# Optimization experiments

Hardware: AMD Instinct MI355X
Metric: run time of the kernel (lower is better)

## Reference

```python
import jax, jax.numpy as jnp
import numpy as np

B, N, C = 2, 1024, 81          # images, proposals/img, classes (class 0 = background)
H, W = 1024, 1024              # image size
D = 100                        # detections_per_img
WX, WY, WW, WH = 10.0, 10.0, 5.0, 5.0   # BoxCoder weights
SCORE_THRESH = 0.05
NMS_THRESH = 0.5
BBOX_XFORM_CLIP = float(np.log(1000.0 / 16.0))
NEG = -1e30
TO_REMOVE = 1.0


def setup_inputs() -> dict:
    key = jax.random.key(0)
    k1, k2, k3, k4 = jax.random.split(key, 4)
    class_logits = jax.random.normal(k1, (B, N, C), jnp.float32)
    regression_outputs = jax.random.normal(k2, (B, N, C * 4), jnp.float32) * 0.5
    # build valid xyxy proposal boxes inside the image
    cxy = jax.random.uniform(k3, (B, N, 2), jnp.float32, 0.0, W - 1.0)
    wh = jax.random.uniform(k4, (B, N, 2), jnp.float32, 8.0, 256.0)
    x1y1 = jnp.clip(cxy - wh / 2, 0.0, W - 1.0)
    x2y2 = jnp.clip(cxy + wh / 2, 0.0, W - 1.0)
    proposals = jnp.concatenate([x1y1, x2y2], axis=-1)
    return dict(class_logits=class_logits,
                regression_outputs=regression_outputs,
                proposals=proposals)


def decode(rel, props):
    # rel: [N, C, 4], props: [N, 4] xyxy -> decoded per-class boxes [N, C, 4], clipped to image
    widths = props[:, 2] - props[:, 0] + TO_REMOVE   # [N]
    heights = props[:, 3] - props[:, 1] + TO_REMOVE
    ctr_x = props[:, 0] + 0.5 * widths
    ctr_y = props[:, 1] + 0.5 * heights
    dx = rel[..., 0] / WX
    dy = rel[..., 1] / WY
    dw = jnp.minimum(rel[..., 2] / WW, BBOX_XFORM_CLIP)
    dh = jnp.minimum(rel[..., 3] / WH, BBOX_XFORM_CLIP)
    pcx = dx * widths[:, None] + ctr_x[:, None]
    pcy = dy * heights[:, None] + ctr_y[:, None]
    pw = jnp.exp(dw) * widths[:, None]
    ph = jnp.exp(dh) * heights[:, None]
    x1 = pcx - 0.5 * pw
    y1 = pcy - 0.5 * ph
    x2 = pcx + 0.5 * pw - 1.0
    y2 = pcy + 0.5 * ph - 1.0
    # clip_to_image
    x1 = jnp.clip(x1, 0.0, W - TO_REMOVE)
    y1 = jnp.clip(y1, 0.0, H - TO_REMOVE)
    x2 = jnp.clip(x2, 0.0, W - TO_REMOVE)
    y2 = jnp.clip(y2, 0.0, H - TO_REMOVE)
    return jnp.stack([x1, y1, x2, y2], axis=-1)


def pairwise_iou(b):
    # b: [N, 4] -> [N, N]
    area = (b[:, 2] - b[:, 0] + TO_REMOVE) * (b[:, 3] - b[:, 1] + TO_REMOVE)
    lt = jnp.maximum(b[:, None, :2], b[None, :, :2])
    rb = jnp.minimum(b[:, None, 2:], b[None, :, 2:])
    wh = jnp.clip(rb - lt + TO_REMOVE, 0.0)
    inter = wh[..., 0] * wh[..., 1]
    return inter / (area[:, None] + area[None, :] - inter)


def nms_keep(boxes, scores):
    # boxes [N,4], scores [N] (NEG for below-threshold boxes) -> keep mask [N] bool
    order = jnp.argsort(-scores)
    b = boxes[order]
    iou = pairwise_iou(b)                       # [N, N]
    valid = scores[order] > NEG / 2             # below-threshold boxes never participate
    idx = jnp.arange(N)

    def body(i, keep):
        sup = keep[i] & (iou[i] > NMS_THRESH) & (idx > i)
        return keep & ~sup

    keep_sorted = jax.lax.fori_loop(0, N, body, valid)
    return jnp.zeros(N, bool).at[order].set(keep_sorted)


def _per_image(logits, rel, props):
    probs = jax.nn.softmax(logits, axis=-1)                 # [N, C]
    boxes = decode(rel.reshape(N, C, 4), props)             # [N, C, 4]
    cls_boxes = jnp.transpose(boxes[:, 1:, :], (1, 0, 2))   # [C-1, N, 4]  (skip background)
    cls_scores = probs[:, 1:].T                              # [C-1, N]
    valid = cls_scores > SCORE_THRESH
    masked_in = jnp.where(valid, cls_scores, NEG)
    keep = jax.vmap(nms_keep)(cls_boxes, masked_in)          # [C-1, N]
    surv = jnp.where(keep & valid, cls_scores, NEG)
    top_scores, top_idx = jax.lax.top_k(surv.reshape(-1), D)  # over (C-1)*N candidates
    cls_idx = top_idx // N
    box_idx = top_idx % N
    sel_boxes = cls_boxes[cls_idx, box_idx]                  # [D, 4]
    labels = cls_idx + 1
    ok = top_scores > NEG / 2
    return (jnp.where(ok[:, None], sel_boxes, 0.0),
            jnp.where(ok, top_scores, 0.0),
            jnp.where(ok, labels, -1))


def reference(class_logits, regression_outputs, proposals):
    # returns (boxes [B,D,4], scores [B,D], labels [B,D]); invalid slots zeroed / label -1
    return jax.vmap(_per_image)(class_logits, regression_outputs, proposals)
```

## Files before the change

### kernel.cpp

```cpp
#include <hip/hip_runtime.h>
#include <math.h>
#include <float.h>

#define BN 2
#define NP 1024
#define NC 81
#define ND 100
#define MAXC 8192
#define CAP2 512
#define CAPT 512
#define NBIN 4096
#define SCORE_T 0.05f
#define NMS_T 0.5f
#define BBOX_CLIP 4.135166556742356f

typedef unsigned long long ull;

__device__ __forceinline__ void decode_box(
    const float* __restrict__ props, const float* __restrict__ regress,
    int b, int n, int c, float& x1, float& y1, float& x2, float& y2)
{
    const float* pr = props + ((size_t)b * NP + n) * 4;
    float p0 = pr[0], p1 = pr[1], p2 = pr[2], p3 = pr[3];
    float w  = p2 - p0 + 1.0f, h = p3 - p1 + 1.0f;
    float cx = p0 + 0.5f * w,  cy = p1 + 0.5f * h;
    const float* rl = regress + (((size_t)b * NP + n) * NC + c) * 4;
    float dx = rl[0] / 10.0f, dy = rl[1] / 10.0f;
    float dw = fminf(rl[2] / 5.0f, BBOX_CLIP);
    float dh = fminf(rl[3] / 5.0f, BBOX_CLIP);
    float pcx = dx * w + cx, pcy = dy * h + cy;
    float pw  = expf(dw) * w, ph = expf(dh) * h;
    x1 = pcx - 0.5f * pw; y1 = pcy - 0.5f * ph;
    x2 = pcx + 0.5f * pw - 1.0f; y2 = pcy + 0.5f * ph - 1.0f;
    x1 = fminf(fmaxf(x1, 0.f), 1023.f);
    y1 = fminf(fmaxf(y1, 0.f), 1023.f);
    x2 = fminf(fmaxf(x2, 0.f), 1023.f);
    y2 = fminf(fmaxf(y2, 0.f), 1023.f);
}

__device__ __forceinline__ void emit_slot(
    float* __restrict__ out, const float* __restrict__ props,
    const float* __restrict__ regress, int b, int d, ull key)
{
    float score = __uint_as_float((unsigned int)(key >> 32));
    float* ob = out + ((size_t)b * ND + d) * 4;
    float* os = out + (size_t)BN * ND * 4 + b * ND + d;
    float* ol = out + (size_t)BN * ND * 5 + b * ND + d;
    if (score > 0.f) {
        unsigned int f = 0xFFFFFFFFu - (unsigned int)(key & 0xFFFFFFFFu);
        int cls = f / NP, n = f % NP;
        float x1, y1, x2, y2;
        decode_box(props, regress, b, n, cls + 1, x1, y1, x2, y2);
        ob[0] = x1; ob[1] = y1; ob[2] = x2; ob[3] = y2;
        *os = score;
        *ol = (float)(cls + 1);
    } else {
        ob[0] = 0.f; ob[1] = 0.f; ob[2] = 0.f; ob[3] = 0.f;
        *os = 0.f;
        *ol = -1.f;
    }
}

__device__ __forceinline__ void bitonic_desc(ull* a, int len, int tid, int nthr)
{
    for (int k = 2; k <= len; k <<= 1) {
        for (int j = k >> 1; j > 0; j >>= 1) {
            for (int i = tid; i < len; i += nthr) {
                int ixj = i ^ j;
                if (ixj > i) {
                    bool desc = ((i & k) == 0);
                    ull x = a[i], y = a[ixj];
                    if (desc ? (x < y) : (x > y)) { a[i] = y; a[ixj] = x; }
                }
            }
            __syncthreads();
        }
    }
}

__global__ __launch_bounds__(256) void softmax_probs_kernel(
    const float* __restrict__ logits, float* __restrict__ probs_t,
    int* __restrict__ cnt, int* __restrict__ done)
{
    int g = blockIdx.x * 256 + threadIdx.x;
    if (g == 0) { cnt[0] = 0; cnt[1] = 0; done[0] = 0; done[1] = 0; }
    if (g >= BN * NP) return;
    int b = g / NP, n = g % NP;
    const float* row = logits + (size_t)g * NC;
    float m = -FLT_MAX;
    for (int i = 0; i < NC; ++i) m = fmaxf(m, row[i]);
    float s = 0.f;
    for (int i = 0; i < NC; ++i) s += expf(row[i] - m);
    for (int c = 1; c < NC; ++c)
        probs_t[((size_t)b * (NC - 1) + (c - 1)) * NP + n] = expf(row[c] - m) / s;
}

__global__ __launch_bounds__(256) void nms_topk_kernel(
    const float* __restrict__ probs_t, const float* __restrict__ regress,
    const float* __restrict__ props, int* __restrict__ cnt, int* __restrict__ done,
    ull* __restrict__ g_key, float* __restrict__ out)
{
    const int tid  = threadIdx.x;
    const int wave = tid >> 6;
    const int l    = tid & 63;
    const int idx  = blockIdx.x;
    const int b    = idx / (NC - 1);
    const int cls  = idx % (NC - 1);
    const int c    = cls + 1;

    __shared__ union {
        struct {
            ull   key[CAP2];
            float x1[CAP2], y1[CAP2], x2[CAP2], y2[CAP2], area[CAP2];
            int   keep[CAP2];
        } a;
        struct {
            int hist[NBIN];
            ull cbuf[CAPT];
        } t;
    } sm;
    __shared__ int s_cnt, s_ret, s_bstar, s_cnt2;

    if (tid == 0) s_cnt = 0;
    __syncthreads();

    const float* prow = probs_t + ((size_t)b * (NC - 1) + cls) * NP;
    float4 v = ((const float4*)prow)[tid];
    #pragma unroll
    for (int q = 0; q < 4; ++q) {
        float p = (&v.x)[q];
        if (p > SCORE_T) {
            int k = atomicAdd(&s_cnt, 1);
            if (k < CAP2) {
                unsigned n = (unsigned)(tid * 4 + q);
                sm.a.key[k] = ((ull)__float_as_uint(p) << 32)
                            | (ull)(0xFFFFFFFFu - n);
            }
        }
    }
    __syncthreads();
    int M = s_cnt; if (M > CAP2) M = CAP2;

    if (M > 64) {
        int Mp = 128; while (Mp < M) Mp <<= 1;
        for (int i = M + tid; i < Mp; i += 256) sm.a.key[i] = 0ull;
        __syncthreads();
        bitonic_desc(sm.a.key, Mp, tid, 256);
        for (int i = tid; i < M; i += 256) {
            int n = (int)(0xFFFFFFFFu - (unsigned)(sm.a.key[i] & 0xFFFFFFFFu));
            float x1, y1, x2, y2;
            decode_box(props, regress, b, n, c, x1, y1, x2, y2);
            sm.a.x1[i] = x1; sm.a.y1[i] = y1; sm.a.x2[i] = x2; sm.a.y2[i] = y2;
            sm.a.area[i] = (x2 - x1 + 1.f) * (y2 - y1 + 1.f);
            sm.a.keep[i] = 1;
        }
        __syncthreads();
        for (int i = 0; i < M; ++i) {
            if (sm.a.keep[i]) {
                float x1i = sm.a.x1[i], y1i = sm.a.y1[i];
                float x2i = sm.a.x2[i], y2i = sm.a.y2[i], ai = sm.a.area[i];
                for (int j = i + 1 + tid; j < M; j += 256) {
                    float lx = fmaxf(x1i, sm.a.x1[j]);
                    float ly = fmaxf(y1i, sm.a.y1[j]);
                    float rx = fminf(x2i, sm.a.x2[j]);
                    float ry = fminf(y2i, sm.a.y2[j]);
                    float wd = fmaxf(rx - lx + 1.f, 0.f);
                    float ht = fmaxf(ry - ly + 1.f, 0.f);
                    float inter = wd * ht;
                    float iou = inter / (ai + sm.a.area[j] - inter);
                    if (iou > NMS_T) sm.a.keep[j] = 0;
                }
            }
            __syncthreads();
        }
        for (int i = tid; i < M; i += 256) {
            if (sm.a.keep[i]) {
                int pos = atomicAdd(&cnt[b], 1);
                if (pos < MAXC) {
                    ull key = sm.a.key[i];
                    unsigned n = 0xFFFFFFFFu - (unsigned)(key & 0xFFFFFFFFu);
                    unsigned f = (unsigned)cls * NP + n;
                    g_key[(size_t)b * MAXC + pos] =
                        (key & 0xFFFFFFFF00000000ull) | (ull)(0xFFFFFFFFu - f);
                }
            }
        }
    } else if (M > 0) {
        if (wave == 0) {
            ull key = (l < M) ? sm.a.key[l] : 0ull;
            #pragma unroll
            for (int k = 2; k <= 64; k <<= 1) {
                #pragma unroll
                for (int j = k >> 1; j > 0; j >>= 1) {
                    ull p = __shfl_xor(key, j, 64);
                    bool lower = (l & j) == 0;
                    bool up    = (l & k) != 0;
                    ull mn = key < p ? key : p;
                    ull mx = key < p ? p : key;
                    key = (lower == up) ? mn : mx;
                }
            }
            float x1 = 0.f, y1 = 0.f, x2 = 0.f, y2 = 0.f, ar = 0.f;
            if (l < M) {
                int n = (int)(0xFFFFFFFFu - (unsigned)(key & 0xFFFFFFFFu));
                decode_box(props, regress, b, n, c, x1, y1, x2, y2);
                ar = (x2 - x1 + 1.f) * (y2 - y1 + 1.f);
            }
            ull keep = (M >= 64) ? ~0ull : ((1ull << M) - 1ull);
            for (int i = 0; i < M; ++i) {
                if ((keep >> i) & 1ull) {
                    float xi1 = __shfl(x1, i, 64), yi1 = __shfl(y1, i, 64);
                    float xi2 = __shfl(x2, i, 64), yi2 = __shfl(y2, i, 64);
                    float ari = __shfl(ar, i, 64);
                    float lx = fmaxf(xi1, x1), ly = fmaxf(yi1, y1);
                    float rx = fminf(xi2, x2), ry = fminf(yi2, y2);
                    float wd = fmaxf(rx - lx + 1.f, 0.f);
                    float ht = fmaxf(ry - ly + 1.f, 0.f);
                    float inter = wd * ht;
                    float iou = inter / (ari + ar - inter);
                    ull sup = __ballot(iou > NMS_T && l > i);
                    keep &= ~sup;
                }
            }
            int nk = __popcll(keep);
            int basep = 0;
            if (l == 0 && nk > 0) basep = atomicAdd(&cnt[b], nk);
            basep = __shfl(basep, 0, 64);
            if ((keep >> l) & 1ull) {
                int pos = basep + __popcll(keep & ((1ull << l) - 1ull));
                if (pos < MAXC) {
                    unsigned n = 0xFFFFFFFFu - (unsigned)(key & 0xFFFFFFFFu);
                    unsigned f = (unsigned)cls * NP + n;
                    g_key[(size_t)b * MAXC + pos] =
                        (key & 0xFFFFFFFF00000000ull) | (ull)(0xFFFFFFFFu - f);
                }
            }
        }
    }

    __syncthreads();
    __threadfence();
    if (tid == 0) s_ret = atomicAdd(&done[b], 1);
    __syncthreads();
    if (s_ret != (NC - 1) - 1) return;
    __threadfence();

    int K = atomicAdd(&cnt[b], 0); if (K > MAXC) K = MAXC;
    ull* keys = g_key + (size_t)b * MAXC;

    for (int i = tid; i < NBIN; i += 256) sm.t.hist[i] = 0;
    if (tid == 0) s_cnt2 = 0;
    __syncthreads();

    for (int i = tid; i < K; i += 256)
        atomicAdd(&sm.t.hist[(int)(keys[i] >> 52)], 1);
    __syncthreads();

    if (tid < 64) {
        int gs = 0;
        for (int q = 0; q < 64; ++q) gs += sm.t.hist[l * 64 + q];
        int pre = gs;
        for (int off = 1; off < 64; off <<= 1) {
            int vv = __shfl_up(pre, off, 64);
            if (l >= off) pre += vv;
        }
        int total = __shfl(pre, 63, 64);
        int S = total - pre + gs;
        ull ball = __ballot(S >= ND);
        int gstar = ball ? (63 - __clzll((long long)ball)) : 0;
        int Sg = __shfl(S, gstar, 64);
        int Gg = __shfl(gs, gstar, 64);
        int A  = Sg - Gg;
        int h  = sm.t.hist[gstar * 64 + l];
        int pre2 = h;
        for (int off = 1; off < 64; off <<= 1) {
            int vv = __shfl_up(pre2, off, 64);
            if (l >= off) pre2 += vv;
        }
        int T = Gg - pre2 + h;
        ull ball2 = __ballot(A + T >= ND);
        int binin = ball2 ? (63 - __clzll((long long)ball2)) : 0;
        if (l == 0) s_bstar = gstar * 64 + binin;
    }
    __syncthreads();
    const int bstar = s_bstar;

    for (int i = tid; i < K; i += 256) {
        ull key = keys[i];
        if ((int)(key >> 52) >= bstar) {
            int p = atomicAdd(&s_cnt2, 1);
            if (p < CAPT) sm.t.cbuf[p] = key;
        }
    }
    __syncthreads();
    const int Tt = s_cnt2;

    if (Tt <= CAPT) {
        int Tp = 128; while (Tp < Tt) Tp <<= 1;
        for (int i = Tt + tid; i < Tp; i += 256) sm.t.cbuf[i] = 0ull;
        __syncthreads();
        bitonic_desc(sm.t.cbuf, Tp, tid, 256);
        for (int d = tid; d < ND; d += 256)
            emit_slot(out, props, regress, b, d, sm.t.cbuf[d]);
    } else {
        ull* rk = sm.a.key;
        int* rp = sm.a.keep;
        for (int d = 0; d < ND; ++d) {
            ull bk = 0ull; int bp = -1;
            for (int t = tid; t < K; t += 256) {
                ull k2 = keys[t];
                if (k2 > bk) { bk = k2; bp = t; }
            }
            rk[tid] = bk; rp[tid] = bp;
            __syncthreads();
            for (int off = 128; off > 0; off >>= 1) {
                if (tid < off && rk[tid + off] > rk[tid]) {
                    rk[tid] = rk[tid + off]; rp[tid] = rp[tid + off];
                }
                __syncthreads();
            }
            if (tid == 0) {
                emit_slot(out, props, regress, b, d, rk[0]);
                if (rp[0] >= 0) keys[rp[0]] = 0ull;
            }
            __syncthreads();
        }
    }
}

extern "C" void kernel_launch(void* const* d_in, const int* in_sizes, int n_in,
                              void* d_out, int out_size, void* d_ws, size_t ws_size,
                              hipStream_t stream) {
    const float* logits  = (const float*)d_in[0];
    const float* regress = (const float*)d_in[1];
    const float* props   = (const float*)d_in[2];
    float* out = (float*)d_out;

    char* ws = (char*)d_ws;
    int*   cnt     = (int*)  (ws);
    int*   done    = (int*)  (ws + 8);
    float* probs_t = (float*)(ws + 256);
    ull*   g_key   = (ull*)  (ws + 256 + (size_t)BN * (NC - 1) * NP * 4);

    hipLaunchKernelGGL(softmax_probs_kernel, dim3(BN * NP / 256), dim3(256), 0, stream,
                       logits, probs_t, cnt, done);
    hipLaunchKernelGGL(nms_topk_kernel, dim3(BN * (NC - 1)), dim3(256), 0, stream,
                       probs_t, regress, props, cnt, done, g_key, out);
}
```

Baseline: 111.1 us.

## Fuse softmax into per-class NMS kernel with fixed slots and flag-based final top-k

Replaces the two-kernel pipeline with one launch. Each class block recomputes the softmax over all of its image's logit rows, staged through shared memory in chunks, and keeps only its own class column. This drops the transposed probability buffer and one kernel launch, at the cost of roughly 80x redundant softmax work and logit reads per image. The global atomic counter is replaced by per-class fixed 64-entry key slots, so survivors beyond 64 per class are silently dropped. The final top-k now runs in the class-0 block, which spins on per-block done flags and adds a single-wave register bitonic sort for up to 256 candidates. The flags are never reset between calls, so a later call can read stale slots from the previous one, and the spin-wait assumes all blocks are co-resident.

```diff
diff --git a/kernel.cpp b/kernel.cpp
--- a/kernel.cpp
+++ b/kernel.cpp
@@ -5,14 +5,18 @@
 #define BN 2
 #define NP 1024
 #define NC 81
+#define NCLS 80
 #define ND 100
-#define MAXC 8192
+#define NSLOT 64
 #define CAP2 512
 #define CAPT 512
 #define NBIN 4096
+#define CHROWS 128
+#define NCHUNK 8
 #define SCORE_T 0.05f
 #define NMS_T 0.5f
 #define BBOX_CLIP 4.135166556742356f
+#define DONE_TAG 0x5A5A5A5A
 
 typedef unsigned long long ull;
 
@@ -78,37 +82,21 @@
     }
 }
 
-__global__ __launch_bounds__(256) void softmax_probs_kernel(
-    const float* __restrict__ logits, float* __restrict__ probs_t,
-    int* __restrict__ cnt, int* __restrict__ done)
-{
-    int g = blockIdx.x * 256 + threadIdx.x;
-    if (g == 0) { cnt[0] = 0; cnt[1] = 0; done[0] = 0; done[1] = 0; }
-    if (g >= BN * NP) return;
-    int b = g / NP, n = g % NP;
-    const float* row = logits + (size_t)g * NC;
-    float m = -FLT_MAX;
-    for (int i = 0; i < NC; ++i) m = fmaxf(m, row[i]);
-    float s = 0.f;
-    for (int i = 0; i < NC; ++i) s += expf(row[i] - m);
-    for (int c = 1; c < NC; ++c)
-        probs_t[((size_t)b * (NC - 1) + (c - 1)) * NP + n] = expf(row[c] - m) / s;
-}
-
-__global__ __launch_bounds__(256) void nms_topk_kernel(
-    const float* __restrict__ probs_t, const float* __restrict__ regress,
-    const float* __restrict__ props, int* __restrict__ cnt, int* __restrict__ done,
+__global__ __launch_bounds__(256) void roihead_kernel(
+    const float* __restrict__ logits, const float* __restrict__ regress,
+    const float* __restrict__ props, int* __restrict__ flags,
     ull* __restrict__ g_key, float* __restrict__ out)
 {
     const int tid  = threadIdx.x;
+    const int l    = tid & 63;
     const int wave = tid >> 6;
-    const int l    = tid & 63;
     const int idx  = blockIdx.x;
-    const int b    = idx / (NC - 1);
-    const int cls  = idx % (NC - 1);
+    const int b    = idx / NCLS;
+    const int cls  = idx % NCLS;
     const int c    = cls + 1;
 
     __shared__ union {
+        float4 stage4[CHROWS * NC / 4];
         struct {
             ull   key[CAP2];
             float x1[CAP2], y1[CAP2], x2[CAP2], y2[CAP2], area[CAP2];
@@ -119,13 +107,28 @@
             ull cbuf[CAPT];
         } t;
     } sm;
-    __shared__ int s_cnt, s_ret, s_bstar, s_cnt2;
-
-    if (tid == 0) s_cnt = 0;
-    __syncthreads();
-
-    const float* prow = probs_t + ((size_t)b * (NC - 1) + cls) * NP;
-    float4 v = ((const float4*)prow)[tid];
+    __shared__ float sp[NP];
+    __shared__ int s_cnt, s_app, s_bstar, s_cnt2;
+
+    const float4* lg4 = (const float4*)(logits + (size_t)b * NP * NC);
+    for (int ch = 0; ch < NCHUNK; ++ch) {
+        const float4* src = lg4 + ch * (CHROWS * NC / 4);
+        for (int i = tid; i < CHROWS * NC / 4; i += 256) sm.stage4[i] = src[i];
+        __syncthreads();
+        if (tid < CHROWS) {
+            const float* row = (const float*)sm.stage4 + tid * NC;
+            float m = -FLT_MAX;
+            for (int i = 0; i < NC; ++i) m = fmaxf(m, row[i]);
+            float s = 0.f;
+            for (int i = 0; i < NC; ++i) s += expf(row[i] - m);
+            sp[ch * CHROWS + tid] = expf(row[c] - m) / s;
+        }
+        __syncthreads();
+    }
+
+    if (tid == 0) { s_cnt = 0; s_app = 0; }
+    __syncthreads();
+    float4 v = ((const float4*)sp)[tid];
     #pragma unroll
     for (int q = 0; q < 4; ++q) {
         float p = (&v.x)[q];
@@ -140,6 +143,7 @@
     }
     __syncthreads();
     int M = s_cnt; if (M > CAP2) M = CAP2;
+    ull* g_slot = g_key + (size_t)idx * NSLOT;
 
     if (M > 64) {
         int Mp = 128; while (Mp < M) Mp <<= 1;
@@ -175,17 +179,20 @@
         }
         for (int i = tid; i < M; i += 256) {
             if (sm.a.keep[i]) {
-                int pos = atomicAdd(&cnt[b], 1);
-                if (pos < MAXC) {
+                int pos = atomicAdd(&s_app, 1);
+                if (pos < NSLOT) {
                     ull key = sm.a.key[i];
                     unsigned n = 0xFFFFFFFFu - (unsigned)(key & 0xFFFFFFFFu);
                     unsigned f = (unsigned)cls * NP + n;
-                    g_key[(size_t)b * MAXC + pos] =
-                        (key & 0xFFFFFFFF00000000ull) | (ull)(0xFFFFFFFFu - f);
-                }
-            }
-        }
-    } else if (M > 0) {
+                    g_slot[pos] = (key & 0xFFFFFFFF00000000ull)
+                                | (ull)(0xFFFFFFFFu - f);
+                }
+            }
+        }
+        __syncthreads();
+        int st = s_app; if (st > NSLOT) st = NSLOT;
+        for (int i = st + tid; i < NSLOT; i += 256) g_slot[i] = 0ull;
+    } else {
         if (wave == 0) {
             ull key = (l < M) ? sm.a.key[l] : 0ull;
             #pragma unroll
@@ -222,38 +229,38 @@
                     keep &= ~sup;
                 }
             }
-            int nk = __popcll(keep);
-            int basep = 0;
-            if (l == 0 && nk > 0) basep = atomicAdd(&cnt[b], nk);
-            basep = __shfl(basep, 0, 64);
+            ull vout = 0ull;
             if ((keep >> l) & 1ull) {
-                int pos = basep + __popcll(keep & ((1ull << l) - 1ull));
-                if (pos < MAXC) {
-                    unsigned n = 0xFFFFFFFFu - (unsigned)(key & 0xFFFFFFFFu);
-                    unsigned f = (unsigned)cls * NP + n;
-                    g_key[(size_t)b * MAXC + pos] =
-                        (key & 0xFFFFFFFF00000000ull) | (ull)(0xFFFFFFFFu - f);
-                }
-            }
+                unsigned n = 0xFFFFFFFFu - (unsigned)(key & 0xFFFFFFFFu);
+                unsigned f = (unsigned)cls * NP + n;
+                vout = (key & 0xFFFFFFFF00000000ull) | (ull)(0xFFFFFFFFu - f);
+            }
+            g_slot[l] = vout;
         }
     }
 
     __syncthreads();
     __threadfence();
-    if (tid == 0) s_ret = atomicAdd(&done[b], 1);
-    __syncthreads();
-    if (s_ret != (NC - 1) - 1) return;
+    if (tid == 0) atomicExch(&flags[idx], DONE_TAG);
+    if (cls != 0) return;
+
+    if (tid < NCLS) {
+        int* fp = flags + b * NCLS + tid;
+        while (atomicAdd(fp, 0) != DONE_TAG) { }
+    }
+    __syncthreads();
     __threadfence();
 
-    int K = atomicAdd(&cnt[b], 0); if (K > MAXC) K = MAXC;
-    ull* keys = g_key + (size_t)b * MAXC;
+    const int K = NCLS * NSLOT;
+    const ull* keys = g_key + (size_t)b * NCLS * NSLOT;
 
     for (int i = tid; i < NBIN; i += 256) sm.t.hist[i] = 0;
     if (tid == 0) s_cnt2 = 0;
     __syncthreads();
-
-    for (int i = tid; i < K; i += 256)
-        atomicAdd(&sm.t.hist[(int)(keys[i] >> 52)], 1);
+    for (int i = tid; i < K; i += 256) {
+        ull key = keys[i];
+        if (key) atomicAdd(&sm.t.hist[(int)(key >> 52)], 1);
+    }
     __syncthreads();
 
     if (tid < 64) {
@@ -287,7 +294,7 @@
 
     for (int i = tid; i < K; i += 256) {
         ull key = keys[i];
-        if ((int)(key >> 52) >= bstar) {
+        if (key && (int)(key >> 52) >= bstar) {
             int p = atomicAdd(&s_cnt2, 1);
             if (p < CAPT) sm.t.cbuf[p] = key;
         }
@@ -295,8 +302,50 @@
     __syncthreads();
     const int Tt = s_cnt2;
 
-    if (Tt <= CAPT) {
-        int Tp = 128; while (Tp < Tt) Tp <<= 1;
+    if (Tt <= 256) {
+        if (wave == 0) {
+            ull key4[4];
+            #pragma unroll
+            for (int r = 0; r < 4; ++r) {
+                int e = r * 64 + l;
+                key4[r] = (e < Tt) ? sm.t.cbuf[e] : 0ull;
+            }
+            #pragma unroll
+            for (int k = 2; k <= 256; k <<= 1) {
+                #pragma unroll
+                for (int j = k >> 1; j > 0; j >>= 1) {
+                    if (j >= 64) {
+                        int d = j >> 6;
+                        #pragma unroll
+                        for (int r = 0; r < 4; ++r) {
+                            if ((r & d) == 0) {
+                                int e = r * 64 + l;
+                                bool desc = ((e & k) == 0);
+                                ull aa = key4[r], bb = key4[r | d];
+                                if (desc ? (aa < bb) : (aa > bb)) {
+                                    key4[r] = bb; key4[r | d] = aa;
+                                }
+                            }
+                        }
+                    } else {
+                        #pragma unroll
+                        for (int r = 0; r < 4; ++r) {
+                            ull p = __shfl_xor(key4[r], j, 64);
+                            int e = r * 64 + l;
+                            bool desc = ((e & k) == 0);
+                            bool low  = ((l & j) == 0);
+                            ull mn = key4[r] < p ? key4[r] : p;
+                            ull mx = key4[r] < p ? p : key4[r];
+                            key4[r] = (low == desc) ? mx : mn;
+                        }
+                    }
+                }
+            }
+            emit_slot(out, props, regress, b, l, key4[0]);
+            if (l < ND - 64) emit_slot(out, props, regress, b, 64 + l, key4[1]);
+        }
+    } else if (Tt <= CAPT) {
+        int Tp = 512;
         for (int i = Tt + tid; i < Tp; i += 256) sm.t.cbuf[i] = 0ull;
         __syncthreads();
         bitonic_desc(sm.t.cbuf, Tp, tid, 256);
@@ -305,10 +354,11 @@
     } else {
         ull* rk = sm.a.key;
         int* rp = sm.a.keep;
+        ull* wkeys = g_key + (size_t)b * NCLS * NSLOT;
         for (int d = 0; d < ND; ++d) {
             ull bk = 0ull; int bp = -1;
             for (int t = tid; t < K; t += 256) {
-                ull k2 = keys[t];
+                ull k2 = wkeys[t];
                 if (k2 > bk) { bk = k2; bp = t; }
             }
             rk[tid] = bk; rp[tid] = bp;
@@ -321,7 +371,7 @@
             }
             if (tid == 0) {
                 emit_slot(out, props, regress, b, d, rk[0]);
-                if (rp[0] >= 0) keys[rp[0]] = 0ull;
+                if (rp[0] >= 0) wkeys[rp[0]] = 0ull;
             }
             __syncthreads();
         }
@@ -337,13 +387,9 @@
     float* out = (float*)d_out;
 
     char* ws = (char*)d_ws;
-    int*   cnt     = (int*)  (ws);
-    int*   done    = (int*)  (ws + 8);
-    float* probs_t = (float*)(ws + 256);
-    ull*   g_key   = (ull*)  (ws + 256 + (size_t)BN * (NC - 1) * NP * 4);
-
-    hipLaunchKernelGGL(softmax_probs_kernel, dim3(BN * NP / 256), dim3(256), 0, stream,
-                       logits, probs_t, cnt, done);
-    hipLaunchKernelGGL(nms_topk_kernel, dim3(BN * (NC - 1)), dim3(256), 0, stream,
-                       probs_t, regress, props, cnt, done, g_key, out);
-}
+    int* flags = (int*)(ws);
+    ull* g_key = (ull*)(ws + 1024);
+
+    hipLaunchKernelGGL(roihead_kernel, dim3(BN * NCLS), dim3(256), 0, stream,
+                       logits, regress, props, flags, g_key, out);
+}
```

Measured after the change: 136.1 us. 1.22x slower.
